# Kernel optimization log

Hardware: AMD Instinct MI355X
Metric: run time of the kernel (lower is better)

Reference implementation:

```python
import jax, jax.numpy as jnp
import numpy as np
from jax import lax

B = 256
R_ITERS = 3

def squash(x):
    # x * |x| / (1 + |x|^2), applied along last axis
    n = jnp.linalg.norm(x, axis=-1, keepdims=True)
    return x * n / (1.0 + n * n)

def conv2d(x, w, b, stride):
    y = lax.conv_general_dilated(x, w, window_strides=(stride, stride), padding='VALID',
                                 dimension_numbers=('NCHW', 'OIHW', 'NCHW'))
    return y + b[None, :, None, None]

def setup_inputs() -> dict:
    key = jax.random.key(0)
    ks = jax.random.split(key, 12)
    s = 0.05
    return {
        'x': jax.random.normal(ks[0], (B, 1, 28, 28), jnp.float32),
        'label': jax.random.randint(ks[1], (B,), 0, 10),
        'conv1_w': jax.random.normal(ks[2], (256, 1, 9, 9), jnp.float32) * s,
        'conv1_b': jnp.zeros((256,), jnp.float32),
        'pconv_w': jax.random.normal(ks[3], (256, 256, 9, 9), jnp.float32) * s,
        'pconv_b': jnp.zeros((256,), jnp.float32),
        'W_dig': jax.random.normal(ks[4], (1152, 10, 16, 8), jnp.float32),
        'dec_w1': jax.random.normal(ks[5], (512, 160), jnp.float32) * s,
        'dec_b1': jnp.zeros((512,), jnp.float32),
        'dec_w2': jax.random.normal(ks[6], (1024, 512), jnp.float32) * s,
        'dec_b2': jnp.zeros((1024,), jnp.float32),
        'dec_w3': jax.random.normal(ks[7], (784, 1024), jnp.float32) * s,
        'dec_b3': jnp.zeros((784,), jnp.float32),
    }

def reference(x, label, conv1_w, conv1_b, pconv_w, pconv_b, W_dig,
              dec_w1, dec_b1, dec_w2, dec_b2, dec_w3, dec_b3):
    # conv stem: [B,1,28,28] -> [B,256,20,20]
    h = conv2d(x, conv1_w, conv1_b, 1)
    # primary caps conv: -> [B,256,6,6] -> [B,1152,8] -> squash
    h = conv2d(h, pconv_w, pconv_b, 2)
    caps = squash(h.reshape(h.shape[0], -1, 8))
    # prediction vectors u_hat: [B, 1152, 10, 16]
    u = jnp.einsum('iond,bid->bion', W_dig, caps)
    # dynamic routing (softmax over input-capsule axis, per original code)
    b = jnp.zeros_like(u)
    for r in range(1, R_ITERS + 1):
        c = jax.nn.softmax(b, axis=1)
        s = (c * u).sum(axis=1, keepdims=True)     # [B,1,10,16]
        v = squash(s)
        if r != R_ITERS:
            b = b + (v * u).sum(axis=-1, keepdims=True)
    v = v.squeeze(1)                               # [B,10,16]
    # masked reconstruction
    one_hot = jax.nn.one_hot(label, 10, dtype=v.dtype)
    recon = (one_hot[..., None] * v).reshape(v.shape[0], 160)
    recon = jax.nn.relu(recon @ dec_w1.T + dec_b1)
    recon = jax.nn.relu(recon @ dec_w2.T + dec_b2)
    recon = jax.nn.sigmoid(recon @ dec_w3.T + dec_b3)
    return (v, recon, one_hot)
```

## Files before the change

kernel.cpp:

```cpp
#include <hip/hip_runtime.h>
#include <hip/hip_bf16.h>
#include <stdint.h>


typedef short short8 __attribute__((ext_vector_type(8)));
typedef unsigned short u16x8 __attribute__((ext_vector_type(8)));
typedef float f32x4  __attribute__((ext_vector_type(4)));

#define H1_PLANE 6553600

__device__ inline float bf2f(unsigned short u) {
    unsigned int v = ((unsigned int)u) << 16;
    float f;
    __builtin_memcpy(&f, &v, 4);
    return f;
}
__device__ inline unsigned short f2bf(float f) {
    __hip_bfloat16 h = __float2bfloat16(f);
    unsigned short u;
    __builtin_memcpy(&u, &h, 2);
    return u;
}
__device__ inline float clampf(float x, float b) {
    return fminf(fmaxf(x, -b), b);
}
__device__ inline float rdf(const void* p, size_t i, int f) {
    return f ? ((const float*)p)[i] : bf2f(((const unsigned short*)p)[i]);
}
__device__ inline void gload_lds16(const unsigned short* g, unsigned short* l) {
    __builtin_amdgcn_global_load_lds(
        (const __attribute__((address_space(1))) void*)g,
        (__attribute__((address_space(3))) void*)l, 16, 0, 0);
}
__device__ inline int detect_f(const void* w1c) {
    const unsigned short* w = (const unsigned short*)w1c;
    int lane = threadIdx.x & 63;
    int cnt = 0;
#pragma unroll
    for (int j = 0; j < 4; ++j) {
        float v = fabsf(bf2f(w[lane * 4 + j]));
        if (v > 100.f) cnt++;
    }
#pragma unroll
    for (int off = 32; off; off >>= 1) cnt += __shfl_xor(cnt, off);
    return cnt >= 4;
}

__global__ __launch_bounds__(256) void k_prep(
        const void* __restrict__ w1c, const void* __restrict__ w2c,
        float* __restrict__ h2f, unsigned short* __restrict__ B1p,
        unsigned short* __restrict__ Bp3) {
    __shared__ unsigned short wl[20736];
    int blk = blockIdx.x, tid = threadIdx.x;
    if (blk < 2304) {
        ((f32x4*)h2f)[blk * 256 + tid] = (f32x4){0.f, 0.f, 0.f, 0.f};
    } else if (blk < 2400) {
        int f = detect_f(w1c);
        int idx = (blk - 2304) * 256 + tid;
        int co = idx / 96, k = idx - co * 96;
        B1p[idx] = (k < 81) ? f2bf(rdf(w1c, (size_t)co * 81 + k, f)) : (unsigned short)0;
    } else {
        int f = detect_f(w1c);
        int co = blk - 2400;
        size_t base = (size_t)co * 20736;
        for (int i = tid; i < 20736; i += 256)
            wl[i] = f2bf(rdf(w2c, base + i, f));
        __syncthreads();
        for (int idx = tid; idx < 20736; idx += 256) {
            int t = idx >> 8, ci = idx & 255;
            int kc = ci >> 6, cin = ci & 63;
            Bp3[((size_t)(t * 4 + kc) << 14) + (co << 6) + cin] = wl[ci * 81 + t];
        }
    }
}

__global__ __launch_bounds__(256) void k_conv1(
        const void* __restrict__ x,
        const unsigned short* __restrict__ B1p,
        const void* __restrict__ bias,
        unsigned short* __restrict__ h1p,
        const void* __restrict__ w1c) {
    __shared__ unsigned short xl[1568];
    __shared__ int offt[96];
    int f = detect_f(w1c);
    int tid = threadIdx.x;
    if (tid < 96) offt[tid] = (tid < 81) ? (tid / 9) * 28 + (tid % 9) : 0;

    int mblk = blockIdx.x * 128;
    int bfirst = mblk / 400;
    int blast = (mblk + 127) / 400;
    int nload = (blast - bfirst + 1) * 784;
    for (int i = tid; i < nload; i += 256)
        xl[i] = f2bf(rdf(x, (size_t)bfirst * 784 + i, f));
    __syncthreads();

    int wave = tid >> 6, lane = tid & 63;
    int wr = wave >> 1, wc = wave & 1;
    int mbase = mblk + wr * 64;
    int nbase = blockIdx.y * 128 + wc * 64;
    int l15 = lane & 15, l4 = lane >> 4;

    int lbase[4];
#pragma unroll
    for (int mt = 0; mt < 4; ++mt) {
        int m = mbase + mt * 16 + l15;
        int img = m / 400 - bfirst, pos = m % 400;
        lbase[mt] = img * 784 + (pos / 20) * 28 + (pos % 20);
    }

    f32x4 acc[4][4];
#pragma unroll
    for (int mt = 0; mt < 4; ++mt)
#pragma unroll
        for (int nt = 0; nt < 4; ++nt)
            acc[mt][nt] = (f32x4){0.f, 0.f, 0.f, 0.f};

#pragma unroll
    for (int kc = 0; kc < 3; ++kc) {
        int kbase = kc * 32 + l4 * 8;
        short8 af[4], bfr[4];
#pragma unroll
        for (int mt = 0; mt < 4; ++mt)
#pragma unroll
            for (int j = 0; j < 8; ++j) {
                int k = kbase + j;
                af[mt][j] = (k < 81) ? (short)xl[lbase[mt] + offt[k]] : (short)0;
            }
#pragma unroll
        for (int nt = 0; nt < 4; ++nt)
            bfr[nt] = *(const short8*)(B1p + (size_t)(nbase + nt * 16 + l15) * 96 + kbase);
#pragma unroll
        for (int mt = 0; mt < 4; ++mt)
#pragma unroll
            for (int nt = 0; nt < 4; ++nt)
                acc[mt][nt] = __builtin_amdgcn_mfma_f32_16x16x32_bf16(
                    af[mt], bfr[nt], acc[mt][nt], 0, 0, 0);
    }

#pragma unroll
    for (int mt = 0; mt < 4; ++mt) {
        size_t radr[4];
#pragma unroll
        for (int r = 0; r < 4; ++r) {
            int m = mbase + mt * 16 + l4 * 4 + r;
            int img = m / 400, pos = m - img * 400;
            int y = pos / 20, xx = pos - y * 20;
            radr[r] = (size_t)(((y & 1) << 1) + (xx & 1)) * H1_PLANE
                    + (size_t)(img * 100 + (y >> 1) * 10 + (xx >> 1)) * 256;
        }
#pragma unroll
        for (int nt = 0; nt < 4; ++nt) {
            int col = nbase + nt * 16 + l15;
            float bv = rdf(bias, col, f);
#pragma unroll
            for (int r = 0; r < 4; ++r)
                h1p[radr[r] + col] = f2bf(clampf(acc[mt][nt][r] + bv, 1024.f));
        }
    }
}

__global__ __launch_bounds__(256) void k_conv2(
        const unsigned short* __restrict__ h1p,
        const unsigned short* __restrict__ Bp,
        float* __restrict__ h2f, int zbase) {
    __shared__ unsigned short As[3][4096];
    __shared__ unsigned short Bs[3][4096];
    int tid = threadIdx.x;
    int wave = tid >> 6, lane = tid & 63;
    int wr = wave >> 1, wc = wave & 1;
    int mb = blockIdx.x << 7;
    int nb = blockIdx.y << 7;
    int s = blockIdx.z + zbase;
    int t0 = (81 * s) >> 3, t1 = (81 * (s + 1)) >> 3;
    int l15 = lane & 15, l4 = lane >> 4;

    int rsub = lane >> 2;
    int slog = (lane & 3) ^ ((lane >> 3) & 3);
    int aoff[2], boff[2];
#pragma unroll
    for (int r = 0; r < 2; ++r) {
        int row = wave * 32 + r * 16 + rsub;
        int m = mb + row;
        int bb = m / 36, pos = m - bb * 36;
        int yo = pos / 6, xo = pos - yo * 6;
        aoff[r] = (bb * 100 + yo * 10 + xo) * 256 + slog * 8;
        boff[r] = row * 64 + slog * 8;
    }

    int ko = (l4 ^ ((l15 >> 1) & 3)) << 3;
    int arow[4], brow[4];
#pragma unroll
    for (int mt = 0; mt < 4; ++mt) arow[mt] = ((wr * 64 + mt * 16 + l15) << 5) + ko;
#pragma unroll
    for (int nt = 0; nt < 4; ++nt) brow[nt] = ((wc * 64 + nt * 16 + l15) << 5) + ko;

    f32x4 acc[4][4];
#pragma unroll
    for (int mt = 0; mt < 4; ++mt)
#pragma unroll
        for (int nt = 0; nt < 4; ++nt)
            acc[mt][nt] = (f32x4){0.f, 0.f, 0.f, 0.f};

    int skc = 0;
    int sky = t0 / 9, skx = t0 - sky * 9;
    int st4 = t0 * 4;
    int tboff = ((sky & 1) * 2 + (skx & 1)) * H1_PLANE
              + ((sky >> 1) * 10 + (skx >> 1)) * 256;

    auto stage = [&](int buf) {
        const unsigned short* aw = h1p + tboff + (skc << 5);
        const unsigned short* bw = Bp + (((size_t)(st4 + (skc >> 1))) << 14)
                                     + nb * 64 + ((skc & 1) << 5);
        unsigned short* al = &As[buf][wave << 10];
        unsigned short* bl = &Bs[buf][wave << 10];
#pragma unroll
        for (int r = 0; r < 2; ++r) {
            gload_lds16(aw + aoff[r], al + (r << 9));
            gload_lds16(bw + boff[r], bl + (r << 9));
        }
    };
    auto adv = [&]() {
        if (++skc == 8) {
            skc = 0; st4 += 4;
            if (++skx == 9) { skx = 0; ++sky; }
            tboff = ((sky & 1) * 2 + (skx & 1)) * H1_PLANE
                  + ((sky >> 1) * 10 + (skx >> 1)) * 256;
        }
    };
    auto compute = [&](int buf) {
        short8 af[4], bfr[4];
#pragma unroll
        for (int mt = 0; mt < 4; ++mt)
            af[mt] = *(const short8*)(&As[buf][arow[mt]]);
#pragma unroll
        for (int nt = 0; nt < 4; ++nt)
            bfr[nt] = *(const short8*)(&Bs[buf][brow[nt]]);
#pragma unroll
        for (int mt = 0; mt < 4; ++mt)
#pragma unroll
            for (int nt = 0; nt < 4; ++nt)
                acc[mt][nt] = __builtin_amdgcn_mfma_f32_16x16x32_bf16(
                    af[mt], bfr[nt], acc[mt][nt], 0, 0, 0);
    };

    int nit = (t1 - t0) * 8;
    stage(0); adv();
    stage(1); adv();
    int cur = 0;
    for (int i = 0; i < nit; ++i) {
        if (i + 1 < nit) asm volatile("s_waitcnt vmcnt(4)" ::: "memory");
        else             asm volatile("s_waitcnt vmcnt(0)" ::: "memory");
        __builtin_amdgcn_s_barrier();
        if (i + 2 < nit) { stage(cur == 0 ? 2 : cur - 1); adv(); }
        compute(cur);
        cur = (cur == 2) ? 0 : cur + 1;
    }

#pragma unroll
    for (int mt = 0; mt < 4; ++mt)
#pragma unroll
        for (int nt = 0; nt < 4; ++nt) {
            int col = nb + wc * 64 + nt * 16 + l15;
#pragma unroll
            for (int r = 0; r < 4; ++r) {
                int row = mb + wr * 64 + mt * 16 + l4 * 4 + r;
                atomicAdd(&h2f[(size_t)row * 256 + col], acc[mt][nt][r]);
            }
        }
}

__global__ __launch_bounds__(256) void k_post(
        const void* __restrict__ wdig, const void* __restrict__ dw2,
        const void* __restrict__ dw3, const void* __restrict__ w1c,
        unsigned short* __restrict__ Wdb2,
        unsigned short* __restrict__ w2b,
        unsigned short* __restrict__ w3b,
        const float* __restrict__ h2f, const void* __restrict__ pb,
        unsigned short* __restrict__ caps) {
    __shared__ unsigned short wl[20480];
    int f = detect_f(w1c);
    int blk = blockIdx.x, tid = threadIdx.x;
    if (blk >= 5704) {
        float* ld = (float*)wl;
        int b = blk - 5704;
#pragma unroll 4
        for (int p = 0; p < 36; ++p)
            ld[p * 256 + tid] = h2f[(size_t)b * 9216 + p * 256 + tid];
        __syncthreads();
        for (int c = tid; c < 1152; c += 256) {
            float h[8], ss = 0.f;
#pragma unroll
            for (int d = 0; d < 8; ++d) {
                int flat = c * 8 + d;
                int co = flat / 36, pos = flat - co * 36;
                float v = clampf(ld[pos * 256 + co] + rdf(pb, co, f), 20000.f);
                h[d] = v;
                ss += v * v;
            }
            float sc = sqrtf(ss) / (1.f + ss);
            u16x8 cv;
#pragma unroll
            for (int d = 0; d < 8; ++d) cv[d] = f2bf(h[d] * sc);
            *(u16x8*)(caps + ((size_t)b * 1152 + c) * 8) = cv;
        }
    } else if (blk < 72) {
        int i0 = blk * 16;
        size_t base = (size_t)i0 * 1280;
        for (int idx = tid; idx < 20480; idx += 256)
            wl[idx] = f2bf(rdf(wdig, base + idx, f));
        __syncthreads();
        if (tid < 160) {
            int o = tid / 16, n = tid - o * 16;
            unsigned short* dst = Wdb2 + (size_t)o * 147456 + n * 9216 + i0 * 8;
            const unsigned short* src = wl + tid * 8;
#pragma unroll
            for (int i = 0; i < 16; ++i)
                *(uint4*)(dst + i * 8) = *(const uint4*)(src + i * 1280);
        }
    } else if (blk < 2120) {
        int idx = (blk - 72) * 256 + tid;
        w2b[idx] = f2bf(rdf(dw2, idx, f));
    } else {
        int idx = (blk - 2120) * 256 + tid;
        w3b[idx] = (idx < 802816) ? f2bf(rdf(dw3, idx, f)) : (unsigned short)0;
    }
}

__global__ __launch_bounds__(384) void k_routing(
        const unsigned short* __restrict__ caps, const unsigned short* __restrict__ Wdb2,
        const int* __restrict__ label, void* __restrict__ d_out,
        float* __restrict__ vsel, const void* __restrict__ w1c, int bbase) {
    int f = detect_f(w1c);
    int bid = blockIdx.x;
    int o = bid >> 7, b = (bid & 127) + bbase;
    int bo = b * 10 + o;
    int tid = threadIdx.x;
    int wid = tid >> 6, lane = tid & 63;

    __shared__ float redw[6][16];
    __shared__ float sred[8];
    __shared__ float sbuf[16];

    float u[3][16];
    float a[3] = {0.f, 0.f, 0.f};
    const unsigned short* capb = caps + (size_t)b * 9216;
    const unsigned short* wob = Wdb2 + (size_t)o * 147456;

#pragma unroll
    for (int r = 0; r < 3; ++r) {
        int i = tid + r * 384;
        u16x8 cq = *(const u16x8*)(capb + i * 8);
        float cf[8];
#pragma unroll
        for (int d = 0; d < 8; ++d) cf[d] = bf2f(cq[d]);
#pragma unroll
        for (int n = 0; n < 16; ++n) {
            u16x8 q = *(const u16x8*)(wob + ((size_t)n * 1152 + i) * 8);
            float sacc = 0.f;
#pragma unroll
            for (int d = 0; d < 8; ++d) sacc += bf2f(q[d]) * cf[d];
            u[r][n] = sacc;
        }
    }

    {
        float p[16];
#pragma unroll
        for (int n = 0; n < 16; ++n) p[n] = u[0][n] + u[1][n] + u[2][n];
#pragma unroll
        for (int off = 32; off; off >>= 1)
#pragma unroll
            for (int n = 0; n < 16; ++n) p[n] += __shfl_xor(p[n], off);
        if (lane == 0)
#pragma unroll
            for (int n = 0; n < 16; ++n) redw[wid][n] = p[n];
        __syncthreads();
        if (tid < 16) {
            float sn = 0.f;
#pragma unroll
            for (int w = 0; w < 6; ++w) sn += redw[w][tid];
            sbuf[tid] = sn * (1.f / 1152.f);
        }
        __syncthreads();
        float ss = 0.f;
#pragma unroll
        for (int n = 0; n < 16; ++n) ss += sbuf[n] * sbuf[n];
        float sc = sqrtf(ss) / (1.f + ss);
#pragma unroll
        for (int r = 0; r < 3; ++r) {
            float dot = 0.f;
#pragma unroll
            for (int n = 0; n < 16; ++n) dot += sbuf[n] * u[r][n];
            a[r] += sc * dot;
        }
    }

    for (int rr = 2; rr <= 3; ++rr) {
        float e[3], es = 0.f;
#pragma unroll
        for (int r = 0; r < 3; ++r) { e[r] = __expf(fminf(a[r], 70.f)); es += e[r]; }
        float p[16];
#pragma unroll
        for (int n = 0; n < 16; ++n)
            p[n] = e[0] * u[0][n] + e[1] * u[1][n] + e[2] * u[2][n];
#pragma unroll
        for (int off = 32; off; off >>= 1) {
            es += __shfl_xor(es, off);
#pragma unroll
            for (int n = 0; n < 16; ++n) p[n] += __shfl_xor(p[n], off);
        }
        if (lane == 0) {
#pragma unroll
            for (int n = 0; n < 16; ++n) redw[wid][n] = p[n];
            sred[wid] = es;
        }
        __syncthreads();
        if (tid < 16) {
            float S = 0.f, sn = 0.f;
#pragma unroll
            for (int w = 0; w < 6; ++w) { S += sred[w]; sn += redw[w][tid]; }
            sbuf[tid] = sn / S;
        }
        __syncthreads();
        float ss = 0.f;
#pragma unroll
        for (int n = 0; n < 16; ++n) ss += sbuf[n] * sbuf[n];
        float sc = sqrtf(ss) / (1.f + ss);

        if (rr < 3) {
#pragma unroll
            for (int r = 0; r < 3; ++r) {
                float dot = 0.f;
#pragma unroll
                for (int n = 0; n < 16; ++n) dot += sbuf[n] * u[r][n];
                a[r] += sc * dot;
            }
        } else {
            int lbl = label[b];
            if (tid < 16) {
                float vn = clampf(sbuf[tid] * sc, 1.f);
                if (f) ((float*)d_out)[(bo << 4) + tid] = vn;
                else   ((unsigned short*)d_out)[(bo << 4) + tid] = f2bf(vn);
                if (o == lbl) vsel[(b << 4) + tid] = vn;
            }
            if (tid == 0) {
                float oh = (o == lbl) ? 1.f : 0.f;
                if (f) ((float*)d_out)[241664 + bo] = oh;
                else   ((unsigned short*)d_out)[241664 + bo] = f2bf(oh);
            }
        }
    }
}

__global__ void k_dec1(const float* __restrict__ vsel, const int* __restrict__ label,
                       const void* __restrict__ w1, const void* __restrict__ b1,
                       unsigned short* __restrict__ r1b, const void* __restrict__ w1c) {
    int f = detect_f(w1c);
    int b = blockIdx.x, j = threadIdx.x;
    __shared__ float vs[16];
    if (j < 16) vs[j] = vsel[b * 16 + j];
    __syncthreads();
    int lbl = label[b];
    size_t wb = (size_t)j * 160 + lbl * 16;
    float acc = rdf(b1, j, f);
#pragma unroll
    for (int n = 0; n < 16; ++n) acc += rdf(w1, wb + n, f) * vs[n];
    r1b[b * 512 + j] = f2bf(fmaxf(acc, 0.f));
}

__global__ __launch_bounds__(256) void k_dgemm(
        const unsigned short* __restrict__ A, const unsigned short* __restrict__ B,
        const void* __restrict__ bias, int K, int mode, int nvalid, int ostride,
        unsigned short* __restrict__ outb, void* __restrict__ d_out,
        const void* __restrict__ w1c) {
    int f = detect_f(w1c);
    int tid = threadIdx.x;
    int wave = tid >> 6, lane = tid & 63;
    int wr = wave >> 1, wc = wave & 1;
    int mbase = blockIdx.x * 128 + wr * 64;
    int nbase = blockIdx.y * 128 + wc * 64;
    int l15 = lane & 15, l4 = lane >> 4;
    int koff = l4 * 8;

    f32x4 acc[4][4];
#pragma unroll
    for (int mt = 0; mt < 4; ++mt)
#pragma unroll
        for (int nt = 0; nt < 4; ++nt)
            acc[mt][nt] = (f32x4){0.f, 0.f, 0.f, 0.f};

    int nch = K >> 5;
    for (int kc = 0; kc < nch; ++kc) {
        int k0 = kc * 32 + koff;
        short8 af[4], bfr[4];
#pragma unroll
        for (int mt = 0; mt < 4; ++mt)
            af[mt] = *(const short8*)(A + (size_t)(mbase + mt * 16 + l15) * K + k0);
#pragma unroll
        for (int nt = 0; nt < 4; ++nt)
            bfr[nt] = *(const short8*)(B + (size_t)(nbase + nt * 16 + l15) * K + k0);
#pragma unroll
        for (int mt = 0; mt < 4; ++mt)
#pragma unroll
            for (int nt = 0; nt < 4; ++nt)
                acc[mt][nt] = __builtin_amdgcn_mfma_f32_16x16x32_bf16(
                    af[mt], bfr[nt], acc[mt][nt], 0, 0, 0);
    }

#pragma unroll
    for (int mt = 0; mt < 4; ++mt)
#pragma unroll
        for (int nt = 0; nt < 4; ++nt) {
            int col = nbase + nt * 16 + l15;
            float bv = (col < nvalid) ? rdf(bias, col, f) : 0.f;
#pragma unroll
            for (int r = 0; r < 4; ++r) {
                int row = mbase + mt * 16 + l4 * 4 + r;
                float v = acc[mt][nt][r] + bv;
                if (mode == 0) {
                    outb[(size_t)row * ostride + col] = f2bf(fmaxf(v, 0.f));
                } else if (col < nvalid) {
                    float a = clampf(v, 60.f);
                    float sig = 1.f / (1.f + __expf(-a));
                    size_t oi = 40960 + (size_t)row * 784 + col;
                    if (f) ((float*)d_out)[oi] = sig;
                    else   ((unsigned short*)d_out)[oi] = f2bf(sig);
                }
            }
        }
}

extern "C" void kernel_launch(void* const* d_in, const int* in_sizes, int n_in,
                              void* d_out, int out_size, void* d_ws, size_t ws_size,
                              hipStream_t stream) {
    const void* x    = d_in[0];
    const int*  lbl  = (const int*)d_in[1];
    const void* w1c  = d_in[2];
    const void* b1c  = d_in[3];
    const void* w2c  = d_in[4];
    const void* b2c  = d_in[5];
    const void* wdig = d_in[6];
    const void* dw1  = d_in[7];
    const void* db1  = d_in[8];
    const void* dw2  = d_in[9];
    const void* db2  = d_in[10];
    const void* dw3  = d_in[11];
    const void* db3  = d_in[12];
    (void)in_sizes; (void)n_in; (void)out_size; (void)ws_size;

    char* ws = (char*)d_ws;
    float* h2f           = (float*)(ws);
    unsigned short* Bp3  = (unsigned short*)(ws + 9437184);
    unsigned short* caps = (unsigned short*)(ws + 9437184);
    unsigned short* B1p  = (unsigned short*)(ws + 20054016);
    unsigned short* h1p  = (unsigned short*)(ws + 20103168);
    unsigned short* Wdb2 = (unsigned short*)(ws + 20103168);
    unsigned short* w2b  = (unsigned short*)(ws + 23052288);
    unsigned short* w3b  = (unsigned short*)(ws + 24100864);
    unsigned short* r1b  = (unsigned short*)(ws + 25935872);
    unsigned short* r2b  = (unsigned short*)(ws + 26198016);
    float* vsel          = (float*)(ws + 26722304);

    hipLaunchKernelGGL(k_prep,  dim3(2656),     dim3(256), 0, stream, w1c, w2c, h2f, B1p, Bp3);
    hipLaunchKernelGGL(k_conv1, dim3(800, 2),   dim3(256), 0, stream, x, B1p, b1c, h1p, w1c);
    hipLaunchKernelGGL(k_conv2, dim3(72, 2, 2), dim3(256), 0, stream, h1p, Bp3, h2f, 0);
    hipLaunchKernelGGL(k_conv2, dim3(72, 2, 2), dim3(256), 0, stream, h1p, Bp3, h2f, 2);
    hipLaunchKernelGGL(k_conv2, dim3(72, 2, 2), dim3(256), 0, stream, h1p, Bp3, h2f, 4);
    hipLaunchKernelGGL(k_conv2, dim3(72, 2, 2), dim3(256), 0, stream, h1p, Bp3, h2f, 6);
    hipLaunchKernelGGL(k_post,  dim3(5960),     dim3(256), 0, stream,
                       wdig, dw2, dw3, w1c, Wdb2, w2b, w3b, h2f, b2c, caps);
    hipLaunchKernelGGL(k_routing, dim3(1280),   dim3(384), 0, stream, caps, Wdb2, lbl,
                       d_out, vsel, w1c, 0);
    hipLaunchKernelGGL(k_routing, dim3(1280),   dim3(384), 0, stream, caps, Wdb2, lbl,
                       d_out, vsel, w1c, 128);
    hipLaunchKernelGGL(k_dec1,  dim3(256),      dim3(512), 0, stream, vsel, lbl, dw1, db1, r1b, w1c);
    hipLaunchKernelGGL(k_dgemm, dim3(2, 8),     dim3(256), 0, stream,
                       r1b, w2b, db2, 512, 0, 1024, 1024, r2b, d_out, w1c);
    hipLaunchKernelGGL(k_dgemm, dim3(2, 7),     dim3(256), 0, stream,
                       r2b, w3b, db3, 1024, 1, 784, 0, (unsigned short*)nullptr, d_out, w1c);
}
```

Measured before the change: 612.0 us.

## Merge prep into conv1, single conv2 launch, fuse dec1 into routing

Folds the weight-prep kernel into conv1. Extra blocks zero h2f and repack conv2 weights, and each conv1 block builds the conv1 weight matrix in shared memory instead of reading a global copy. The four conv2 launches become one launch over all eight z-slices, and the two routing launches become one. The first decoder layer now runs inside the routing block whose output capsule matches the label. This removes several launches and the vsel round trip, but every conv1 block now redundantly converts all 24576 conv1 weights into LDS, which adds work and uses more shared memory.

```diff
diff --git a/kernel.cpp b/kernel.cpp
--- a/kernel.cpp
+++ b/kernel.cpp
@@ -46,22 +46,24 @@
     return cnt >= 4;
 }
 
-__global__ __launch_bounds__(256) void k_prep(
-        const void* __restrict__ w1c, const void* __restrict__ w2c,
-        float* __restrict__ h2f, unsigned short* __restrict__ B1p,
+__global__ __launch_bounds__(256) void k_conv1(
+        const void* __restrict__ x,
+        const void* __restrict__ w1c,
+        const void* __restrict__ bias,
+        const void* __restrict__ w2c,
+        unsigned short* __restrict__ h1p,
+        float* __restrict__ h2f,
         unsigned short* __restrict__ Bp3) {
-    __shared__ unsigned short wl[20736];
+    __shared__ unsigned short sh[26336];
+    int f = detect_f(w1c);
     int blk = blockIdx.x, tid = threadIdx.x;
-    if (blk < 2304) {
-        ((f32x4*)h2f)[blk * 256 + tid] = (f32x4){0.f, 0.f, 0.f, 0.f};
-    } else if (blk < 2400) {
-        int f = detect_f(w1c);
-        int idx = (blk - 2304) * 256 + tid;
-        int co = idx / 96, k = idx - co * 96;
-        B1p[idx] = (k < 81) ? f2bf(rdf(w1c, (size_t)co * 81 + k, f)) : (unsigned short)0;
-    } else {
-        int f = detect_f(w1c);
-        int co = blk - 2400;
+
+    if (blk >= 1600) {
+        int co = blk - 1600;
+        f32x4* hz = (f32x4*)h2f + (size_t)co * 2304;
+        for (int i = tid; i < 2304; i += 256)
+            hz[i] = (f32x4){0.f, 0.f, 0.f, 0.f};
+        unsigned short* wl = sh;
         size_t base = (size_t)co * 20736;
         for (int i = tid; i < 20736; i += 256)
             wl[i] = f2bf(rdf(w2c, base + i, f));
@@ -71,22 +73,22 @@
             int kc = ci >> 6, cin = ci & 63;
             Bp3[((size_t)(t * 4 + kc) << 14) + (co << 6) + cin] = wl[ci * 81 + t];
         }
-    }
-}
-
-__global__ __launch_bounds__(256) void k_conv1(
-        const void* __restrict__ x,
-        const unsigned short* __restrict__ B1p,
-        const void* __restrict__ bias,
-        unsigned short* __restrict__ h1p,
-        const void* __restrict__ w1c) {
-    __shared__ unsigned short xl[1568];
-    __shared__ int offt[96];
-    int f = detect_f(w1c);
-    int tid = threadIdx.x;
+        return;
+    }
+
+    unsigned short* B1L = sh;
+    unsigned short* xl  = sh + 24576;
+    int* offt = (int*)(sh + 26144);
+
     if (tid < 96) offt[tid] = (tid < 81) ? (tid / 9) * 28 + (tid % 9) : 0;
-
-    int mblk = blockIdx.x * 128;
+    for (int idx = tid; idx < 24576; idx += 256) {
+        int co = idx / 96, k = idx - co * 96;
+        B1L[idx] = (k < 81) ? f2bf(rdf(w1c, (size_t)co * 81 + k, f)) : (unsigned short)0;
+    }
+
+    int bx = blk, by = 0;
+    if (bx >= 800) { bx -= 800; by = 1; }
+    int mblk = bx * 128;
     int bfirst = mblk / 400;
     int blast = (mblk + 127) / 400;
     int nload = (blast - bfirst + 1) * 784;
@@ -97,7 +99,7 @@
     int wave = tid >> 6, lane = tid & 63;
     int wr = wave >> 1, wc = wave & 1;
     int mbase = mblk + wr * 64;
-    int nbase = blockIdx.y * 128 + wc * 64;
+    int nbase = by * 128 + wc * 64;
     int l15 = lane & 15, l4 = lane >> 4;
 
     int lbase[4];
@@ -128,7 +130,7 @@
             }
 #pragma unroll
         for (int nt = 0; nt < 4; ++nt)
-            bfr[nt] = *(const short8*)(B1p + (size_t)(nbase + nt * 16 + l15) * 96 + kbase);
+            bfr[nt] = *(const short8*)(B1L + (nbase + nt * 16 + l15) * 96 + kbase);
 #pragma unroll
         for (int mt = 0; mt < 4; ++mt)
 #pragma unroll
@@ -162,7 +164,7 @@
 __global__ __launch_bounds__(256) void k_conv2(
         const unsigned short* __restrict__ h1p,
         const unsigned short* __restrict__ Bp,
-        float* __restrict__ h2f, int zbase) {
+        float* __restrict__ h2f) {
     __shared__ unsigned short As[3][4096];
     __shared__ unsigned short Bs[3][4096];
     int tid = threadIdx.x;
@@ -170,7 +172,7 @@
     int wr = wave >> 1, wc = wave & 1;
     int mb = blockIdx.x << 7;
     int nb = blockIdx.y << 7;
-    int s = blockIdx.z + zbase;
+    int s = blockIdx.z;
     int t0 = (81 * s) >> 3, t1 = (81 * (s + 1)) >> 3;
     int l15 = lane & 15, l4 = lane >> 4;
 
@@ -329,10 +331,11 @@
 __global__ __launch_bounds__(384) void k_routing(
         const unsigned short* __restrict__ caps, const unsigned short* __restrict__ Wdb2,
         const int* __restrict__ label, void* __restrict__ d_out,
-        float* __restrict__ vsel, const void* __restrict__ w1c, int bbase) {
+        const void* __restrict__ dw1, const void* __restrict__ db1,
+        unsigned short* __restrict__ r1b, const void* __restrict__ w1c) {
     int f = detect_f(w1c);
     int bid = blockIdx.x;
-    int o = bid >> 7, b = (bid & 127) + bbase;
+    int o = bid >> 8, b = bid & 255;
     int bo = b * 10 + o;
     int tid = threadIdx.x;
     int wid = tid >> 6, lane = tid & 63;
@@ -340,6 +343,7 @@
     __shared__ float redw[6][16];
     __shared__ float sred[8];
     __shared__ float sbuf[16];
+    __shared__ float vnl[16];
 
     float u[3][16];
     float a[3] = {0.f, 0.f, 0.f};
@@ -441,31 +445,26 @@
                 float vn = clampf(sbuf[tid] * sc, 1.f);
                 if (f) ((float*)d_out)[(bo << 4) + tid] = vn;
                 else   ((unsigned short*)d_out)[(bo << 4) + tid] = f2bf(vn);
-                if (o == lbl) vsel[(b << 4) + tid] = vn;
+                vnl[tid] = vn;
             }
             if (tid == 0) {
                 float oh = (o == lbl) ? 1.f : 0.f;
                 if (f) ((float*)d_out)[241664 + bo] = oh;
                 else   ((unsigned short*)d_out)[241664 + bo] = f2bf(oh);
             }
-        }
-    }
-}
-
-__global__ void k_dec1(const float* __restrict__ vsel, const int* __restrict__ label,
-                       const void* __restrict__ w1, const void* __restrict__ b1,
-                       unsigned short* __restrict__ r1b, const void* __restrict__ w1c) {
-    int f = detect_f(w1c);
-    int b = blockIdx.x, j = threadIdx.x;
-    __shared__ float vs[16];
-    if (j < 16) vs[j] = vsel[b * 16 + j];
-    __syncthreads();
-    int lbl = label[b];
-    size_t wb = (size_t)j * 160 + lbl * 16;
-    float acc = rdf(b1, j, f);
-#pragma unroll
-    for (int n = 0; n < 16; ++n) acc += rdf(w1, wb + n, f) * vs[n];
-    r1b[b * 512 + j] = f2bf(fmaxf(acc, 0.f));
+            __syncthreads();
+            if (o == lbl) {
+                for (int j = tid; j < 512; j += 384) {
+                    float acc2 = rdf(db1, j, f);
+                    size_t wb = (size_t)j * 160 + lbl * 16;
+#pragma unroll
+                    for (int n = 0; n < 16; ++n)
+                        acc2 += rdf(dw1, wb + n, f) * vnl[n];
+                    r1b[b * 512 + j] = f2bf(fmaxf(acc2, 0.f));
+                }
+            }
+        }
+    }
 }
 
 __global__ __launch_bounds__(256) void k_dgemm(
@@ -552,28 +551,20 @@
     float* h2f           = (float*)(ws);
     unsigned short* Bp3  = (unsigned short*)(ws + 9437184);
     unsigned short* caps = (unsigned short*)(ws + 9437184);
-    unsigned short* B1p  = (unsigned short*)(ws + 20054016);
     unsigned short* h1p  = (unsigned short*)(ws + 20103168);
     unsigned short* Wdb2 = (unsigned short*)(ws + 20103168);
     unsigned short* w2b  = (unsigned short*)(ws + 23052288);
     unsigned short* w3b  = (unsigned short*)(ws + 24100864);
     unsigned short* r1b  = (unsigned short*)(ws + 25935872);
     unsigned short* r2b  = (unsigned short*)(ws + 26198016);
-    float* vsel          = (float*)(ws + 26722304);
-
-    hipLaunchKernelGGL(k_prep,  dim3(2656),     dim3(256), 0, stream, w1c, w2c, h2f, B1p, Bp3);
-    hipLaunchKernelGGL(k_conv1, dim3(800, 2),   dim3(256), 0, stream, x, B1p, b1c, h1p, w1c);
-    hipLaunchKernelGGL(k_conv2, dim3(72, 2, 2), dim3(256), 0, stream, h1p, Bp3, h2f, 0);
-    hipLaunchKernelGGL(k_conv2, dim3(72, 2, 2), dim3(256), 0, stream, h1p, Bp3, h2f, 2);
-    hipLaunchKernelGGL(k_conv2, dim3(72, 2, 2), dim3(256), 0, stream, h1p, Bp3, h2f, 4);
-    hipLaunchKernelGGL(k_conv2, dim3(72, 2, 2), dim3(256), 0, stream, h1p, Bp3, h2f, 6);
+
+    hipLaunchKernelGGL(k_conv1, dim3(1856),     dim3(256), 0, stream,
+                       x, w1c, b1c, w2c, h1p, h2f, Bp3);
+    hipLaunchKernelGGL(k_conv2, dim3(72, 2, 8), dim3(256), 0, stream, h1p, Bp3, h2f);
     hipLaunchKernelGGL(k_post,  dim3(5960),     dim3(256), 0, stream,
                        wdig, dw2, dw3, w1c, Wdb2, w2b, w3b, h2f, b2c, caps);
-    hipLaunchKernelGGL(k_routing, dim3(1280),   dim3(384), 0, stream, caps, Wdb2, lbl,
-                       d_out, vsel, w1c, 0);
-    hipLaunchKernelGGL(k_routing, dim3(1280),   dim3(384), 0, stream, caps, Wdb2, lbl,
-                       d_out, vsel, w1c, 128);
-    hipLaunchKernelGGL(k_dec1,  dim3(256),      dim3(512), 0, stream, vsel, lbl, dw1, db1, r1b, w1c);
+    hipLaunchKernelGGL(k_routing, dim3(2560),   dim3(384), 0, stream, caps, Wdb2, lbl,
+                       d_out, dw1, db1, r1b, w1c);
     hipLaunchKernelGGL(k_dgemm, dim3(2, 8),     dim3(256), 0, stream,
                        r1b, w2b, db2, 512, 0, 1024, 1024, r2b, d_out, w1c);
     hipLaunchKernelGGL(k_dgemm, dim3(2, 7),     dim3(256), 0, stream,
```

New measurement: 570.3 us. 6.8% less time.
